# Kernel tuning notes

Hardware: AMD Instinct MI355X
Metric: run time of the kernel (lower is better)

The kernel has to match this reference:

```python
import math
import jax, jax.numpy as jnp
import numpy as np

NUM_HEADS = 4
HEAD_DIM = 384


def reshape_fortran(x, shape):
    # column-major (Fortran) reshape, matching the torch reverse-permute trick
    x = jnp.transpose(x, tuple(reversed(range(x.ndim))))
    x = x.reshape(tuple(reversed(shape)))
    return jnp.transpose(x, tuple(reversed(range(len(shape)))))


def rel_pos_rotate(data):
    # data: [b, n_heads, L=2M-1, S] -> [b, n_heads, S, S]
    data = jnp.transpose(data, (0, 2, 3, 1))  # [b, d0=L, d1=S, d2=H]
    b, d0, d1, d2 = data.shape
    data = jnp.concatenate([data, jnp.zeros((b, d1, d1, d2), data.dtype)], axis=1)
    data = reshape_fortran(data, (b, (d0 + d1) * d1, 1, d2))
    data = data[:, :(d1 + d0 - 1) * d1]
    data = reshape_fortran(data, (b, d0 + d1 - 1, d1, d2))
    n = d0 // 2
    data = jnp.swapaxes(data[:, n:n + d1], 1, 2)  # [b, d1, d1, d2]
    return jnp.transpose(data, (0, 3, 1, 2))      # [b, H, S, S]


def setup_inputs() -> dict:
    key = jax.random.key(0)
    ks = jax.random.split(key, 5)
    B, S, D = 4, 920, 1536
    M = 920
    return {
        "hidden_states": jax.random.normal(ks[0], (B, S, D), jnp.float32),
        "q_w": jax.random.normal(ks[1], (D, NUM_HEADS * HEAD_DIM), jnp.float32) * 0.02,
        "k_w": jax.random.normal(ks[2], (D, NUM_HEADS * HEAD_DIM), jnp.float32) * 0.02,
        "v_w": jax.random.normal(ks[3], (D, NUM_HEADS * HEAD_DIM), jnp.float32) * 0.02,
        "dist_emb": jax.random.normal(ks[4], (2 * M - 1, HEAD_DIM), jnp.float32) * 0.02,
    }


def reference(hidden_states, q_w, k_w, v_w, dist_emb):
    B, S, D = hidden_states.shape

    def heads(x):  # [B,S,H*hd] -> [B,H,S,hd]
        return jnp.transpose(x.reshape(B, S, NUM_HEADS, HEAD_DIM), (0, 2, 1, 3))

    # query is pre-scaled by 1/sqrt(head_dim), matching the torch code
    q = heads((hidden_states @ q_w) / math.sqrt(HEAD_DIM))
    k = heads(hidden_states @ k_w)
    v = heads(hidden_states @ v_w)

    scores = jnp.einsum("bhqd,bhkd->bhqk", q, k)  # [B,H,S,S]
    # relative position scores: [B,H,L,S] then skew-rotated into [B,H,S,S]
    rel = jnp.einsum("ld,bhsd->bhls", dist_emb, q)
    scores = scores + rel_pos_rotate(rel)

    probs = jax.nn.softmax(scores, axis=-1)
    ctx = jnp.einsum("bhqk,bhkd->bhqd", probs, v)  # [B,H,S,hd]
    ctx = jnp.transpose(ctx, (0, 2, 1, 3)).reshape(B, S, NUM_HEADS * HEAD_DIM)
    return ctx
```

## Files before the change

kernel.cpp:

```cpp
#include <hip/hip_runtime.h>
#include <cstdint>
#include <cstddef>

#define SEQ   920
#define DM    1536
#define DH    384
#define NHD   4
#define NB    4
#define NBH   16
#define MTOK  3680
#define NREL  1839

typedef short          bf16x8 __attribute__((ext_vector_type(8)));
typedef float          f32x4  __attribute__((ext_vector_type(4)));
typedef unsigned short u16x4  __attribute__((ext_vector_type(4)));
typedef unsigned short u16x8  __attribute__((ext_vector_type(8)));

__device__ __forceinline__ unsigned short f2bf(float f){
  union{float f; unsigned u;} v; v.f = f;
  unsigned r = v.u + 0x7FFFu + ((v.u >> 16) & 1u);
  return (unsigned short)(r >> 16);
}
__device__ __forceinline__ float bf2f(unsigned short h){
  union{unsigned u; float f;} v; v.u = ((unsigned)h) << 16;
  return v.f;
}
__device__ __forceinline__ f32x4 mfma_bf16(bf16x8 a, bf16x8 b, f32x4 c){
  return __builtin_amdgcn_mfma_f32_16x16x32_bf16(a, b, c, 0, 0, 0);
}
__device__ __forceinline__ void gload_lds16(const void* g, void* l){
  __builtin_amdgcn_global_load_lds((const __attribute__((address_space(1))) void*)g,
                                   (__attribute__((address_space(3))) void*)l, 16, 0, 0);
}

__global__ __launch_bounds__(256) void k_prep(const float* __restrict__ X,
                                              const float* __restrict__ de,
                                              const float* __restrict__ qw,
                                              const float* __restrict__ kw,
                                              const float* __restrict__ vw,
                                              unsigned short* __restrict__ Xb,
                                              unsigned short* __restrict__ Eb,
                                              unsigned short* __restrict__ Wt){
  __shared__ float t[32][33];
  int bid = blockIdx.x;
  if(bid < 6912){
    int z = bid / 2304, rem = bid % 2304;
    int k0 = (rem % 48) * 32, n0 = (rem / 48) * 32;
    const float* w = z == 0 ? qw : (z == 1 ? kw : vw);
    int tx = threadIdx.x & 31, ty = threadIdx.x >> 5;
    #pragma unroll
    for(int j = 0; j < 4; j++)
      t[ty*4+j][tx] = w[(size_t)(k0 + ty*4 + j) * DM + n0 + tx];
    __syncthreads();
    #pragma unroll
    for(int j = 0; j < 4; j++)
      Wt[(size_t)(z*DM + n0 + ty*4 + j) * DM + k0 + tx] = f2bf(t[tx][ty*4+j]);
  } else if(bid < 6912 + 2048){
    int i = ((bid - 6912) * 256 + threadIdx.x) * 4;
    const int n = MTOK*DM, stride = 2048 * 256 * 4;
    for(; i + 3 < n; i += stride){
      f32x4 v = *(const f32x4*)(X + i);
      u16x4 o; o.x = f2bf(v.x); o.y = f2bf(v.y); o.z = f2bf(v.z); o.w = f2bf(v.w);
      *(u16x4*)(Xb + i) = o;
    }
  } else {
    int i = ((bid - 6912 - 2048) * 256 + threadIdx.x) * 4;
    if(i + 3 < NREL*DH){
      f32x4 v = *(const f32x4*)(de + i);
      u16x4 o; o.x = f2bf(v.x); o.y = f2bf(v.y); o.z = f2bf(v.z); o.w = f2bf(v.w);
      *(u16x4*)(Eb + i) = o;
    }
  }
}

template<class Epi>
__device__ __forceinline__ void gemm384(const unsigned short* __restrict__ A, int lda, int Amax,
                                        const unsigned short* __restrict__ B, int ldb, int Bmax,
                                        int K, int m0, int n0, Epi epi){
  __shared__ char lds[147456];
  char* ldsA = lds;
  char* ldsB = lds + 98304;
  const int tid = threadIdx.x;
  const int w = tid >> 6, l = tid & 63;
  const int lg = l >> 4, lo = l & 15;
  const int wm = w >> 1, wn = w & 1;

  const int gcol = ((tid & 7) ^ ((tid >> 3) & 7)) * 16;
  const char* gA[6]; const char* gB[3];
  #pragma unroll
  for(int u = 0; u < 6; u++){
    int ar = m0 + u*64 + (tid >> 3); ar = ar < Amax ? ar : Amax - 1;
    gA[u] = (const char*)A + (size_t)ar*lda*2 + gcol;
  }
  #pragma unroll
  for(int v = 0; v < 3; v++){
    int br = n0 + v*64 + (tid >> 3); br = br < Bmax ? br : Bmax - 1;
    gB[v] = (const char*)B + (size_t)br*ldb*2 + gcol;
  }
  auto stage_all = [&](int kt, int s){
    size_t koff = (size_t)kt * 128;
    #pragma unroll
    for(int u = 0; u < 6; u++)
      gload_lds16(gA[u] + koff, ldsA + s*49152 + u*8192 + tid*16);
    #pragma unroll
    for(int v = 0; v < 3; v++)
      gload_lds16(gB[v] + koff, ldsB + s*24576 + v*8192 + tid*16);
  };

  f32x4 acc[6][6] = {};
  const int sw = (lo & 7) << 4;
  const int nk = K >> 6;

  stage_all(0, 0);
  asm volatile("s_waitcnt vmcnt(0)" ::: "memory");
  __builtin_amdgcn_s_barrier();

  for(int t = 0; t < nk; t++){
    const int s = t & 1, sn = s ^ 1;
    const bool pf = (t + 1 < nk);
    const char* Ab = ldsA + s*49152;
    const char* Bb = ldsB + s*24576;
    if(pf) stage_all(t + 1, sn);

    bf16x8 b0[6], b1[6], a0[3], a1[3];
    #pragma unroll
    for(int fj = 0; fj < 6; fj++){
      b0[fj] = *(const bf16x8*)(Bb + (wn*96 + fj*16 + lo)*128 + ((lg*16) ^ sw));
      b1[fj] = *(const bf16x8*)(Bb + (wn*96 + fj*16 + lo)*128 + ((64 + lg*16) ^ sw));
    }
    #pragma unroll
    for(int fi = 0; fi < 3; fi++){
      a0[fi] = *(const bf16x8*)(Ab + (wm*96 + fi*16 + lo)*128 + ((lg*16) ^ sw));
      a1[fi] = *(const bf16x8*)(Ab + (wm*96 + fi*16 + lo)*128 + ((64 + lg*16) ^ sw));
    }
    __builtin_amdgcn_s_setprio(1);
    #pragma unroll
    for(int fi = 0; fi < 3; fi++)
      #pragma unroll
      for(int fj = 0; fj < 6; fj++)
        acc[fi][fj] = mfma_bf16(a0[fi], b0[fj], acc[fi][fj]);
    #pragma unroll
    for(int fi = 0; fi < 3; fi++)
      #pragma unroll
      for(int fj = 0; fj < 6; fj++)
        acc[fi][fj] = mfma_bf16(a1[fi], b1[fj], acc[fi][fj]);
    __builtin_amdgcn_s_setprio(0);

    #pragma unroll
    for(int fi = 0; fi < 3; fi++){
      a0[fi] = *(const bf16x8*)(Ab + (wm*96 + (fi+3)*16 + lo)*128 + ((lg*16) ^ sw));
      a1[fi] = *(const bf16x8*)(Ab + (wm*96 + (fi+3)*16 + lo)*128 + ((64 + lg*16) ^ sw));
    }
    __builtin_amdgcn_s_setprio(1);
    #pragma unroll
    for(int fi = 0; fi < 3; fi++)
      #pragma unroll
      for(int fj = 0; fj < 6; fj++)
        acc[fi+3][fj] = mfma_bf16(a0[fi], b0[fj], acc[fi+3][fj]);
    #pragma unroll
    for(int fi = 0; fi < 3; fi++)
      #pragma unroll
      for(int fj = 0; fj < 6; fj++)
        acc[fi+3][fj] = mfma_bf16(a1[fi], b1[fj], acc[fi+3][fj]);
    __builtin_amdgcn_s_setprio(0);

    if(pf){
      asm volatile("s_waitcnt vmcnt(0)" ::: "memory");
      __builtin_amdgcn_s_barrier();
    }
  }

  #pragma unroll
  for(int fi = 0; fi < 6; fi++)
    #pragma unroll
    for(int fj = 0; fj < 6; fj++){
      int m = m0 + wm*96 + fi*16 + lg*4;
      int n = n0 + wn*96 + fj*16 + lo;
      epi(m, n, acc[fi][fj]);
    }
}

template<int NF, class Epi>
__device__ __forceinline__ void gemm192(const unsigned short* __restrict__ A, int lda, int Amax,
                                        const unsigned short* __restrict__ B, int ldb, int Bmax,
                                        int K, int m0, int n0, Epi epi){
  __shared__ unsigned short As[3*192*64];
  __shared__ unsigned short Bs[3*64*NF*64];
  const int tid = threadIdx.x;
  const int w = tid >> 6, l = tid & 63;
  const int lg = l >> 4, lo = l & 15;
  const int wm = w >> 2, wn = w & 3;
  const int BSLOT = 8192*NF;

  const char* ga[3]; const char* gb[NF];
  #pragma unroll
  for(int r = 0; r < 3; r++){
    int row = r*64 + (tid >> 3);
    int gslot = (tid & 7) ^ (row & 7);
    int ar = m0 + row; ar = ar < Amax ? ar : Amax - 1;
    ga[r] = (const char*)A + (size_t)ar*lda*2 + gslot*16;
  }
  #pragma unroll
  for(int r = 0; r < NF; r++){
    int row = r*64 + (tid >> 3);
    int gslot = (tid & 7) ^ (row & 7);
    int br = n0 + row; br = br < Bmax ? br : Bmax - 1;
    gb[r] = (const char*)B + (size_t)br*ldb*2 + gslot*16;
  }
  const int ldst = tid * 16;

  auto stage_pair = [&](int kt, int slot, int r){
    size_t koff = (size_t)kt * 128;
    gload_lds16(ga[r] + koff, (char*)As + slot*24576 + r*8192 + ldst);
    if(r < NF)
      gload_lds16(gb[r] + koff, (char*)Bs + slot*BSLOT + r*8192 + ldst);
  };
  auto wait_steady = [&]{
    if constexpr(NF == 3) asm volatile("s_waitcnt vmcnt(6)" ::: "memory");
    else                  asm volatile("s_waitcnt vmcnt(5)" ::: "memory");
  };

  f32x4 acc[6][NF] = {};
  const int sw = (lo & 7) << 4;
  const int nk = (2*K + 127) >> 7;
  const int tb = 2*K - (nk - 1)*128;
  const bool keep0 = (lg*16) < tb;
  const bool keep1 = (64 + lg*16) < tb;

  #pragma unroll
  for(int r = 0; r < 3; r++) stage_pair(0, 0, r);
  #pragma unroll
  for(int r = 0; r < 3; r++) stage_pair(1, 1, r);
  wait_steady();
  __builtin_amdgcn_s_barrier();

  int st = 0;
  for(int t = 0; t < nk; t++){
    const bool last = (t == nk - 1);
    const bool pf = (t + 2 < nk);
    const int s2 = st + 2 >= 3 ? st - 1 : st + 2;
    const char* Ab = (const char*)As + st*24576;
    const char* Bb = (const char*)Bs + st*BSLOT;

    bf16x8 bfr[NF][2], afr[2][2];

    #pragma unroll
    for(int fj = 0; fj < NF; fj++){
      int row = wn*(16*NF) + fj*16 + lo;
      #pragma unroll
      for(int kk = 0; kk < 2; kk++)
        bfr[fj][kk] = *(const bf16x8*)(Bb + row*128 + ((kk*64 + lg*16) ^ sw));
    }
    #pragma unroll
    for(int fi = 0; fi < 2; fi++){
      int row = wm*96 + fi*16 + lo;
      #pragma unroll
      for(int kk = 0; kk < 2; kk++)
        afr[fi][kk] = *(const bf16x8*)(Ab + row*128 + ((kk*64 + lg*16) ^ sw));
    }
    if(pf) stage_pair(t + 2, s2, 0);
    if(last){
      #pragma unroll
      for(int fi = 0; fi < 2; fi++){
        if(!keep0) afr[fi][0] = bf16x8{};
        if(!keep1) afr[fi][1] = bf16x8{};
      }
    }
    __builtin_amdgcn_s_barrier();
    asm volatile("s_waitcnt lgkmcnt(0)" ::: "memory");
    __builtin_amdgcn_s_setprio(1);
    #pragma unroll
    for(int kk = 0; kk < 2; kk++)
      #pragma unroll
      for(int fi = 0; fi < 2; fi++)
        #pragma unroll
        for(int fj = 0; fj < NF; fj++)
          acc[fi][fj] = mfma_bf16(afr[fi][kk], bfr[fj][kk], acc[fi][fj]);
    __builtin_amdgcn_s_setprio(0);
    __builtin_amdgcn_s_barrier();

    #pragma unroll
    for(int fi = 0; fi < 2; fi++){
      int row = wm*96 + (fi + 2)*16 + lo;
      #pragma unroll
      for(int kk = 0; kk < 2; kk++)
        afr[fi][kk] = *(const bf16x8*)(Ab + row*128 + ((kk*64 + lg*16) ^ sw));
    }
    if(pf) stage_pair(t + 2, s2, 1);
    if(last){
      #pragma unroll
      for(int fi = 0; fi < 2; fi++){
        if(!keep0) afr[fi][0] = bf16x8{};
        if(!keep1) afr[fi][1] = bf16x8{};
      }
    }
    __builtin_amdgcn_s_barrier();
    asm volatile("s_waitcnt lgkmcnt(0)" ::: "memory");
    __builtin_amdgcn_s_setprio(1);
    #pragma unroll
    for(int kk = 0; kk < 2; kk++)
      #pragma unroll
      for(int fi = 0; fi < 2; fi++)
        #pragma unroll
        for(int fj = 0; fj < NF; fj++)
          acc[fi + 2][fj] = mfma_bf16(afr[fi][kk], bfr[fj][kk], acc[fi + 2][fj]);
    __builtin_amdgcn_s_setprio(0);
    __builtin_amdgcn_s_barrier();

    #pragma unroll
    for(int fi = 0; fi < 2; fi++){
      int row = wm*96 + (fi + 4)*16 + lo;
      #pragma unroll
      for(int kk = 0; kk < 2; kk++)
        afr[fi][kk] = *(const bf16x8*)(Ab + row*128 + ((kk*64 + lg*16) ^ sw));
    }
    if(pf){
      stage_pair(t + 2, s2, 2);
      wait_steady();
    } else if(t + 1 < nk){
      asm volatile("s_waitcnt vmcnt(0)" ::: "memory");
    }
    if(last){
      #pragma unroll
      for(int fi = 0; fi < 2; fi++){
        if(!keep0) afr[fi][0] = bf16x8{};
        if(!keep1) afr[fi][1] = bf16x8{};
      }
    }
    __builtin_amdgcn_s_barrier();
    asm volatile("s_waitcnt lgkmcnt(0)" ::: "memory");
    __builtin_amdgcn_s_setprio(1);
    #pragma unroll
    for(int kk = 0; kk < 2; kk++)
      #pragma unroll
      for(int fi = 0; fi < 2; fi++)
        #pragma unroll
        for(int fj = 0; fj < NF; fj++)
          acc[fi + 4][fj] = mfma_bf16(afr[fi][kk], bfr[fj][kk], acc[fi + 4][fj]);
    __builtin_amdgcn_s_setprio(0);
    __builtin_amdgcn_s_barrier();

    st = st + 1 >= 3 ? 0 : st + 1;
  }

  #pragma unroll
  for(int fi = 0; fi < 6; fi++)
    #pragma unroll
    for(int fj = 0; fj < NF; fj++){
      int m = m0 + wm*96 + fi*16 + lg*4;
      int n = n0 + wn*(16*NF) + fj*16 + lo;
      epi(m, n, acc[fi][fj]);
    }
}

template<class Epi>
__device__ __forceinline__ void gemm256(const unsigned short* __restrict__ A, int lda, int Amax,
                                        const unsigned short* __restrict__ B, int ldb, int Bmax,
                                        int K, int m0, int n0, Epi epi){
  __shared__ char lds[131072];
  char* ldsA = lds;
  char* ldsB = lds + 65536;
  const int tid = threadIdx.x;
  const int w = tid >> 6, l = tid & 63;
  const int lg = l >> 4, lo = l & 15;
  const int wm = w >> 2, wn = w & 3;

  const int gcol = ((tid & 7) ^ ((tid >> 3) & 7)) * 16;
  const char* gA[2][2]; const char* gB[2][2];
  #pragma unroll
  for(int u = 0; u < 2; u++)
    #pragma unroll
    for(int j = 0; j < 2; j++){
      int ar = m0 + u*128 + j*64 + (tid >> 3); ar = ar < Amax ? ar : Amax - 1;
      gA[u][j] = (const char*)A + (size_t)ar*lda*2 + gcol;
      int br = n0 + u*128 + j*64 + (tid >> 3); br = br < Bmax ? br : Bmax - 1;
      gB[u][j] = (const char*)B + (size_t)br*ldb*2 + gcol;
    }
  auto stageA = [&](int kt, int s, int u){
    size_t koff = (size_t)kt * 128;
    #pragma unroll
    for(int j = 0; j < 2; j++)
      gload_lds16(gA[u][j] + koff, ldsA + s*32768 + u*16384 + j*8192 + tid*16);
  };
  auto stageB = [&](int kt, int s, int u){
    size_t koff = (size_t)kt * 128;
    #pragma unroll
    for(int j = 0; j < 2; j++)
      gload_lds16(gB[u][j] + koff, ldsB + s*32768 + u*16384 + j*8192 + tid*16);
  };

  f32x4 acc[2][4][4] = {};
  const int sw = (lo & 7) << 4;
  const int nk = K >> 6;

  stageB(0, 0, 0); stageB(0, 0, 1); stageA(0, 0, 0); stageA(0, 0, 1);
  asm volatile("s_waitcnt vmcnt(2)" ::: "memory");
  __builtin_amdgcn_s_barrier();

  for(int t = 0; t < nk; t++){
    const int s = t & 1, sn = s ^ 1;
    const bool pf = (t + 1 < nk);
    const char* Ab = ldsA + s*32768;
    const char* Bb = ldsB + s*32768;
    bf16x8 b0[4], b1[4], ar[4];

    #pragma unroll
    for(int fj = 0; fj < 4; fj++)
      b0[fj] = *(const bf16x8*)(Bb + (wn*64 + fj*16 + lo)*128 + ((lg*16) ^ sw));
    #pragma unroll
    for(int fi = 0; fi < 4; fi++)
      ar[fi] = *(const bf16x8*)(Ab + (wm*64 + fi*16 + lo)*128 + ((lg*16) ^ sw));
    if(pf) stageB(t + 1, sn, 0);
    __builtin_amdgcn_s_barrier();
    asm volatile("s_waitcnt lgkmcnt(0)" ::: "memory");
    __builtin_amdgcn_s_setprio(1);
    #pragma unroll
    for(int fi = 0; fi < 4; fi++)
      #pragma unroll
      for(int fj = 0; fj < 4; fj++)
        acc[0][fi][fj] = mfma_bf16(ar[fi], b0[fj], acc[0][fi][fj]);
    __builtin_amdgcn_s_setprio(0);

    #pragma unroll
    for(int fj = 0; fj < 4; fj++)
      b1[fj] = *(const bf16x8*)(Bb + (wn*64 + fj*16 + lo)*128 + ((64 + lg*16) ^ sw));
    #pragma unroll
    for(int fi = 0; fi < 4; fi++)
      ar[fi] = *(const bf16x8*)(Ab + (wm*64 + fi*16 + lo)*128 + ((64 + lg*16) ^ sw));
    if(pf){ stageB(t + 1, sn, 1);
            asm volatile("s_waitcnt vmcnt(4)" ::: "memory"); }
    else  { asm volatile("s_waitcnt vmcnt(0)" ::: "memory"); }
    __builtin_amdgcn_s_barrier();
    asm volatile("s_waitcnt lgkmcnt(0)" ::: "memory");
    __builtin_amdgcn_s_setprio(1);
    #pragma unroll
    for(int fi = 0; fi < 4; fi++)
      #pragma unroll
      for(int fj = 0; fj < 4; fj++)
        acc[0][fi][fj] = mfma_bf16(ar[fi], b1[fj], acc[0][fi][fj]);
    __builtin_amdgcn_s_setprio(0);

    #pragma unroll
    for(int fi = 0; fi < 4; fi++)
      ar[fi] = *(const bf16x8*)(Ab + (128 + wm*64 + fi*16 + lo)*128 + ((lg*16) ^ sw));
    if(pf) stageA(t + 1, sn, 0);
    __builtin_amdgcn_s_barrier();
    asm volatile("s_waitcnt lgkmcnt(0)" ::: "memory");
    __builtin_amdgcn_s_setprio(1);
    #pragma unroll
    for(int fi = 0; fi < 4; fi++)
      #pragma unroll
      for(int fj = 0; fj < 4; fj++)
        acc[1][fi][fj] = mfma_bf16(ar[fi], b0[fj], acc[1][fi][fj]);
    __builtin_amdgcn_s_setprio(0);

    #pragma unroll
    for(int fi = 0; fi < 4; fi++)
      ar[fi] = *(const bf16x8*)(Ab + (128 + wm*64 + fi*16 + lo)*128 + ((64 + lg*16) ^ sw));
    if(pf){ stageA(t + 1, sn, 1);
            asm volatile("s_waitcnt vmcnt(2)" ::: "memory"); }
    __builtin_amdgcn_s_barrier();
    asm volatile("s_waitcnt lgkmcnt(0)" ::: "memory");
    __builtin_amdgcn_s_setprio(1);
    #pragma unroll
    for(int fi = 0; fi < 4; fi++)
      #pragma unroll
      for(int fj = 0; fj < 4; fj++)
        acc[1][fi][fj] = mfma_bf16(ar[fi], b1[fj], acc[1][fi][fj]);
    __builtin_amdgcn_s_setprio(0);
  }

  #pragma unroll
  for(int lh = 0; lh < 2; lh++)
    #pragma unroll
    for(int fi = 0; fi < 4; fi++)
      #pragma unroll
      for(int fj = 0; fj < 4; fj++){
        int m = m0 + lh*128 + wm*64 + fi*16 + lg*4;
        int n = n0 + wn*64 + fj*16 + lo;
        epi(m, n, acc[lh][fi][fj]);
      }
}

__global__ __launch_bounds__(512, 2) void k_proj(const unsigned short* __restrict__ X,
                                                 const unsigned short* __restrict__ Wt,
                                                 unsigned short* __restrict__ Qb,
                                                 unsigned short* __restrict__ Kb,
                                                 unsigned short* __restrict__ Vt){
  int bid = blockIdx.x;
  int wg  = (bid & 7) * 30 + (bid >> 3);
  int m0 = (wg % 10) * 384, n0 = (wg / 10) * 192;
  gemm384(X, DM, MTOK, Wt, DM, 3*DM, DM, m0, n0,
    [=] __device__ (int m, int n, f32x4 v4){
      if(m >= MTOK) return;
      int which = n / DM, r = n % DM, h = r / DH, d = r % DH;
      int b = m / SEQ, s = m % SEQ;
      int bh = b * NHD + h;
      if(which == 2){
        u16x4 o;
        o.x = f2bf(v4.x); o.y = f2bf(v4.y); o.z = f2bf(v4.z); o.w = f2bf(v4.w);
        *(u16x4*)(Vt + ((size_t)bh*DH + d)*SEQ + s) = o;
      } else if(which == 0){
        #pragma unroll
        for(int i = 0; i < 4; i++)
          Qb[((size_t)bh*SEQ + s + i)*DH + d] = f2bf(v4[i] * 0.05103103630798287f);
      } else {
        #pragma unroll
        for(int i = 0; i < 4; i++)
          Kb[((size_t)bh*SEQ + s + i)*DH + d] = f2bf(v4[i]);
      }
    });
}

__global__ __launch_bounds__(512) void k_rel(const unsigned short* __restrict__ Qb,
                                             const unsigned short* __restrict__ E,
                                             unsigned short* __restrict__ relS){
  int m0 = blockIdx.x * 192, n0 = blockIdx.y * 192;
  int s0 = m0 % SEQ;
  int qlo = s0, qhi = s0 + 191;
  if(qhi >= SEQ){ qlo = 0; qhi = SEQ - 1; }
  if(n0 + 191 < 919 - qhi || n0 > 1838 - qlo) return;
  gemm192<3>(Qb, DH, NBH*SEQ, E, DH, NREL, DH, m0, n0,
    [=] __device__ (int m, int n, f32x4 v4){
      #pragma unroll
      for(int i = 0; i < 4; i++){
        int mi = m + i;
        if(mi >= NBH*SEQ) continue;
        int q = mi % SEQ;
        int j = n - 919 + q;
        if(j < 0 || j >= SEQ) continue;
        relS[(size_t)mi*SEQ + j] = f2bf(v4[i]);
      }
    });
}

__global__ __launch_bounds__(512, 2) void k_sgemm(const unsigned short* __restrict__ Qb,
                                                  const unsigned short* __restrict__ Kb,
                                                  unsigned short* __restrict__ P,
                                                  float* __restrict__ rs2){
  __shared__ float rsLds[256];
  if(threadIdx.x < 256) rsLds[threadIdx.x] = 0.f;
  int bid = blockIdx.x;
  int wg = (bid & 7) * 32 + (bid >> 3);
  int bh = wg >> 4, r = wg & 15;
  int m0 = (r & 3) * 256, n0 = (r >> 2) * 256;
  const unsigned short* A = Qb + (size_t)bh*SEQ*DH;
  const unsigned short* B = Kb + (size_t)bh*SEQ*DH;
  unsigned short* Pbh = P + (size_t)bh*SEQ*SEQ;
  const int lo = threadIdx.x & 15;
  gemm256(A, DH, SEQ, B, DH, SEQ, DH, m0, n0,
    [=] __device__ (int m, int n, f32x4 v4){
      float s[4];
      #pragma unroll
      for(int i = 0; i < 4; i++){
        int mi = m + i;
        float p = 0.f;
        if(mi < SEQ && n < SEQ){
          size_t off = (size_t)mi*SEQ + n;
          p = __expf(v4[i] + bf2f(Pbh[off]));
          Pbh[off] = f2bf(p);
        }
        s[i] = p;
      }
      #pragma unroll
      for(int i = 0; i < 4; i++){
        float v = s[i];
        v += __shfl_xor(v, 1); v += __shfl_xor(v, 2);
        v += __shfl_xor(v, 4); v += __shfl_xor(v, 8);
        if(lo == 0) atomicAdd(&rsLds[m - m0 + i], v);
      }
    });
  __syncthreads();
  if(threadIdx.x < 256){
    int row = m0 + threadIdx.x;
    if(row < SEQ) rs2[(((size_t)(n0 >> 8))*NBH + bh)*SEQ + row] = rsLds[threadIdx.x];
  }
}

__global__ __launch_bounds__(512) void k_pv(const unsigned short* __restrict__ P,
                                            const unsigned short* __restrict__ Vt,
                                            const float* __restrict__ rs2,
                                            float* __restrict__ out){
  int bid = blockIdx.x;
  int wg = (bid & 7) * 30 + (bid >> 3);
  int bh = wg / 15, r = wg % 15;
  int m0 = (r % 5) * 192, n0 = (r / 5) * 128;
  const unsigned short* A = P  + (size_t)bh*SEQ*SEQ;
  const unsigned short* B = Vt + (size_t)bh*DH*SEQ;
  const int b = bh >> 2, h = bh & 3;
  gemm192<2>(A, SEQ, SEQ, B, SEQ, DH, SEQ, m0, n0,
    [=] __device__ (int m, int n, f32x4 v4){
      #pragma unroll
      for(int i = 0; i < 4; i++){
        int mi = m + i;
        if(mi >= SEQ) continue;
        float den = rs2[(size_t)bh*SEQ + mi]
                  + rs2[((size_t)1*NBH + bh)*SEQ + mi]
                  + rs2[((size_t)2*NBH + bh)*SEQ + mi]
                  + rs2[((size_t)3*NBH + bh)*SEQ + mi];
        out[((size_t)(b*SEQ + mi))*DM + h*DH + n] = v4[i] / den;
      }
    });
}

extern "C" void kernel_launch(void* const* d_in, const int* in_sizes, int n_in,
                              void* d_out, int out_size, void* d_ws, size_t ws_size,
                              hipStream_t stream){
  const float* X  = (const float*)d_in[0];
  const float* qw = (const float*)d_in[1];
  const float* kw = (const float*)d_in[2];
  const float* vw = (const float*)d_in[3];
  const float* de = (const float*)d_in[4];
  float* out = (float*)d_out;
  char* ws = (char*)d_ws;

  unsigned short* Qb   = (unsigned short*)ws;
  unsigned short* Kb   = (unsigned short*)(ws + 11304960);
  unsigned short* Vt   = (unsigned short*)(ws + 22609920);
  unsigned short* relS = (unsigned short*)(ws + 33914880);
  unsigned short* Eb   = (unsigned short*)(ws + 60999680);
  unsigned short* Xb   = (unsigned short*)(ws + 33914880);
  unsigned short* Wt   = (unsigned short*)(ws + 45219840);
  float*          rs2  = (float*)(ws + 60999680);

  k_prep<<<dim3(9650), dim3(256), 0, stream>>>(X, de, qw, kw, vw, Xb, Eb, Wt);
  k_proj<<<dim3(240), dim3(512), 0, stream>>>(Xb, Wt, Qb, Kb, Vt);
  k_rel<<<dim3(77,10), dim3(512), 0, stream>>>(Qb, Eb, relS);
  k_sgemm<<<dim3(256), dim3(512), 0, stream>>>(Qb, Kb, relS, rs2);
  k_pv<<<dim3(240), dim3(512), 0, stream>>>(relS, Vt, rs2, out);
}
```

Measured before the change: 203.9 us.

## Retile projection GEMM to 192x192 tiles with 3-stage LDS pipeline

The QKV projection GEMM moves from 384x192 tiles on 512-thread blocks to 192x192 tiles on 256-thread blocks, launching 480 blocks instead of 240. The K step shrinks to 32, and a triple-buffered LDS ring keeps two stages of global-to-LDS loads in flight, with a matching swizzle. The aim is better CU fill on the 256-CU part and smaller LDS use, so more blocks can be resident and load latency overlaps compute. The cost is more barriers per K step and less reuse per tile, so more redundant global reads.

```diff
diff --git a/kernel.cpp b/kernel.cpp
--- a/kernel.cpp
+++ b/kernel.cpp
@@ -74,100 +74,74 @@
 }
 
 template<class Epi>
-__device__ __forceinline__ void gemm384(const unsigned short* __restrict__ A, int lda, int Amax,
-                                        const unsigned short* __restrict__ B, int ldb, int Bmax,
-                                        int K, int m0, int n0, Epi epi){
-  __shared__ char lds[147456];
-  char* ldsA = lds;
-  char* ldsB = lds + 98304;
+__device__ __forceinline__ void gemm192w4(const unsigned short* __restrict__ A, int lda, int Amax,
+                                          const unsigned short* __restrict__ B, int ldb, int Bmax,
+                                          int K, int m0, int n0, Epi epi){
+  __shared__ char As[3*12288];
+  __shared__ char Bs[3*12288];
   const int tid = threadIdx.x;
   const int w = tid >> 6, l = tid & 63;
   const int lg = l >> 4, lo = l & 15;
   const int wm = w >> 1, wn = w & 1;
 
-  const int gcol = ((tid & 7) ^ ((tid >> 3) & 7)) * 16;
-  const char* gA[6]; const char* gB[3];
-  #pragma unroll
-  for(int u = 0; u < 6; u++){
-    int ar = m0 + u*64 + (tid >> 3); ar = ar < Amax ? ar : Amax - 1;
-    gA[u] = (const char*)A + (size_t)ar*lda*2 + gcol;
-  }
-  #pragma unroll
-  for(int v = 0; v < 3; v++){
-    int br = n0 + v*64 + (tid >> 3); br = br < Bmax ? br : Bmax - 1;
-    gB[v] = (const char*)B + (size_t)br*ldb*2 + gcol;
-  }
-  auto stage_all = [&](int kt, int s){
-    size_t koff = (size_t)kt * 128;
-    #pragma unroll
-    for(int u = 0; u < 6; u++)
-      gload_lds16(gA[u] + koff, ldsA + s*49152 + u*8192 + tid*16);
-    #pragma unroll
-    for(int v = 0; v < 3; v++)
-      gload_lds16(gB[v] + koff, ldsB + s*24576 + v*8192 + tid*16);
+  const int gslot = ((tid & 3) ^ ((tid >> 3) & 3)) * 16;
+  const char* ga[3]; const char* gb[3];
+  #pragma unroll
+  for(int j = 0; j < 3; j++){
+    int ar = m0 + j*64 + (tid >> 2); ar = ar < Amax ? ar : Amax - 1;
+    ga[j] = (const char*)A + (size_t)ar*lda*2 + gslot;
+    int br = n0 + j*64 + (tid >> 2); br = br < Bmax ? br : Bmax - 1;
+    gb[j] = (const char*)B + (size_t)br*ldb*2 + gslot;
+  }
+  auto stage = [&](int kt, int slot){
+    size_t koff = (size_t)kt * 64;
+    #pragma unroll
+    for(int j = 0; j < 3; j++){
+      gload_lds16(ga[j] + koff, As + slot*12288 + j*4096 + tid*16);
+      gload_lds16(gb[j] + koff, Bs + slot*12288 + j*4096 + tid*16);
+    }
   };
 
   f32x4 acc[6][6] = {};
-  const int sw = (lo & 7) << 4;
-  const int nk = K >> 6;
-
-  stage_all(0, 0);
-  asm volatile("s_waitcnt vmcnt(0)" ::: "memory");
+  const int sw = ((lo >> 1) & 3) << 4;
+  const int nk = K >> 5;
+
+  stage(0, 0);
+  stage(1, 1);
+  asm volatile("s_waitcnt vmcnt(6)" ::: "memory");
   __builtin_amdgcn_s_barrier();
 
+  int st = 0;
   for(int t = 0; t < nk; t++){
-    const int s = t & 1, sn = s ^ 1;
-    const bool pf = (t + 1 < nk);
-    const char* Ab = ldsA + s*49152;
-    const char* Bb = ldsB + s*24576;
-    if(pf) stage_all(t + 1, sn);
-
-    bf16x8 b0[6], b1[6], a0[3], a1[3];
-    #pragma unroll
-    for(int fj = 0; fj < 6; fj++){
-      b0[fj] = *(const bf16x8*)(Bb + (wn*96 + fj*16 + lo)*128 + ((lg*16) ^ sw));
-      b1[fj] = *(const bf16x8*)(Bb + (wn*96 + fj*16 + lo)*128 + ((64 + lg*16) ^ sw));
-    }
-    #pragma unroll
-    for(int fi = 0; fi < 3; fi++){
-      a0[fi] = *(const bf16x8*)(Ab + (wm*96 + fi*16 + lo)*128 + ((lg*16) ^ sw));
-      a1[fi] = *(const bf16x8*)(Ab + (wm*96 + fi*16 + lo)*128 + ((64 + lg*16) ^ sw));
-    }
-    __builtin_amdgcn_s_setprio(1);
-    #pragma unroll
-    for(int fi = 0; fi < 3; fi++)
+    const bool pf = (t + 2 < nk);
+    const int s2 = st + 2 >= 3 ? st - 1 : st + 2;
+    const char* Ab = As + st*12288;
+    const char* Bb = Bs + st*12288;
+
+    bf16x8 a[6], b[6];
+    #pragma unroll
+    for(int fi = 0; fi < 6; fi++)
+      a[fi] = *(const bf16x8*)(Ab + (wm*96 + fi*16 + lo)*64 + ((lg*16) ^ sw));
+    #pragma unroll
+    for(int fj = 0; fj < 6; fj++)
+      b[fj] = *(const bf16x8*)(Bb + (wn*96 + fj*16 + lo)*64 + ((lg*16) ^ sw));
+    if(pf) stage(t + 2, s2);
+    __builtin_amdgcn_s_barrier();
+    asm volatile("s_waitcnt lgkmcnt(0)" ::: "memory");
+    __builtin_amdgcn_s_setprio(1);
+    #pragma unroll
+    for(int fi = 0; fi < 6; fi++)
       #pragma unroll
       for(int fj = 0; fj < 6; fj++)
-        acc[fi][fj] = mfma_bf16(a0[fi], b0[fj], acc[fi][fj]);
-    #pragma unroll
-    for(int fi = 0; fi < 3; fi++)
-      #pragma unroll
-      for(int fj = 0; fj < 6; fj++)
-        acc[fi][fj] = mfma_bf16(a1[fi], b1[fj], acc[fi][fj]);
-    __builtin_amdgcn_s_setprio(0);
-
-    #pragma unroll
-    for(int fi = 0; fi < 3; fi++){
-      a0[fi] = *(const bf16x8*)(Ab + (wm*96 + (fi+3)*16 + lo)*128 + ((lg*16) ^ sw));
-      a1[fi] = *(const bf16x8*)(Ab + (wm*96 + (fi+3)*16 + lo)*128 + ((64 + lg*16) ^ sw));
-    }
-    __builtin_amdgcn_s_setprio(1);
-    #pragma unroll
-    for(int fi = 0; fi < 3; fi++)
-      #pragma unroll
-      for(int fj = 0; fj < 6; fj++)
-        acc[fi+3][fj] = mfma_bf16(a0[fi], b0[fj], acc[fi+3][fj]);
-    #pragma unroll
-    for(int fi = 0; fi < 3; fi++)
-      #pragma unroll
-      for(int fj = 0; fj < 6; fj++)
-        acc[fi+3][fj] = mfma_bf16(a1[fi], b1[fj], acc[fi+3][fj]);
-    __builtin_amdgcn_s_setprio(0);
-
+        acc[fi][fj] = mfma_bf16(a[fi], b[fj], acc[fi][fj]);
+    __builtin_amdgcn_s_setprio(0);
     if(pf){
+      asm volatile("s_waitcnt vmcnt(6)" ::: "memory");
+    } else if(t + 1 < nk){
       asm volatile("s_waitcnt vmcnt(0)" ::: "memory");
-      __builtin_amdgcn_s_barrier();
-    }
+    }
+    __builtin_amdgcn_s_barrier();
+    st = st + 1 >= 3 ? 0 : st + 1;
   }
 
   #pragma unroll
@@ -482,15 +456,15 @@
       }
 }
 
-__global__ __launch_bounds__(512, 2) void k_proj(const unsigned short* __restrict__ X,
+__global__ __launch_bounds__(256, 2) void k_proj(const unsigned short* __restrict__ X,
                                                  const unsigned short* __restrict__ Wt,
                                                  unsigned short* __restrict__ Qb,
                                                  unsigned short* __restrict__ Kb,
                                                  unsigned short* __restrict__ Vt){
   int bid = blockIdx.x;
-  int wg  = (bid & 7) * 30 + (bid >> 3);
-  int m0 = (wg % 10) * 384, n0 = (wg / 10) * 192;
-  gemm384(X, DM, MTOK, Wt, DM, 3*DM, DM, m0, n0,
+  int wg  = (bid & 7) * 60 + (bid >> 3);
+  int m0 = (wg % 20) * 192, n0 = (wg / 20) * 192;
+  gemm192w4(X, DM, MTOK, Wt, DM, 3*DM, DM, m0, n0,
     [=] __device__ (int m, int n, f32x4 v4){
       if(m >= MTOK) return;
       int which = n / DM, r = n % DM, h = r / DH, d = r % DH;
@@ -624,7 +598,7 @@
   float*          rs2  = (float*)(ws + 60999680);
 
   k_prep<<<dim3(9650), dim3(256), 0, stream>>>(X, de, qw, kw, vw, Xb, Eb, Wt);
-  k_proj<<<dim3(240), dim3(512), 0, stream>>>(Xb, Wt, Qb, Kb, Vt);
+  k_proj<<<dim3(480), dim3(256), 0, stream>>>(Xb, Wt, Qb, Kb, Vt);
   k_rel<<<dim3(77,10), dim3(512), 0, stream>>>(Qb, Eb, relS);
   k_sgemm<<<dim3(256), dim3(512), 0, stream>>>(Qb, Kb, relS, rs2);
   k_pv<<<dim3(240), dim3(512), 0, stream>>>(relS, Vt, rs2, out);
```

After: 211.3 us. 1.04x slower.
